# Optimization experiments

Hardware: AMD Instinct MI355X
Metric: run time of the kernel (lower is better)

Reference implementation:

```python
import jax, jax.numpy as jnp
import numpy as np

B, DIM, H, W = 8, 512, 32, 32
NUM_HEADS, KEY_DIM, VALUE_DIM, DIM_OUT = 8, 64, 64, 512


def setup_inputs() -> dict:
    key = jax.random.key(0)
    ks = jax.random.split(key, 5)
    return {
        "x": jax.random.normal(ks[0], (B, DIM, H, W), dtype=jnp.float32),
        "query_proj": jax.random.normal(ks[1], (NUM_HEADS, KEY_DIM, DIM), dtype=jnp.float32),
        "key_proj": jax.random.normal(ks[2], (DIM, KEY_DIM), dtype=jnp.float32),
        "value_proj": jax.random.normal(ks[3], (DIM, VALUE_DIM), dtype=jnp.float32),
        "out_proj": jax.random.normal(ks[4], (DIM_OUT, NUM_HEADS, VALUE_DIM), dtype=jnp.float32),
    }


def reference(x, query_proj, key_proj, value_proj, out_proj):
    b, d, h, w = x.shape
    key_dim = query_proj.shape[1]
    scale = key_dim ** (-0.5)
    # flatten spatial dims to tokens: [b, n, d] where n = h*w (m == x here)
    rx = jnp.transpose(x.reshape(b, d, h * w), (0, 2, 1))
    q = jnp.einsum('bnd,hkd->bnhk', rx, query_proj)
    k = jnp.einsum('bmd,dk->bmk', rx, key_proj)          # single shared K head
    attn = jax.nn.softmax(jnp.einsum('bnhk,bmk->bnhm', q, k) * scale, axis=-1)
    v = jnp.einsum('bmd,dv->bmv', rx, value_proj)        # single shared V head
    o = jnp.einsum('bnhm,bmv->bnhv', attn, v)
    result = jnp.einsum('bnhv,dhv->bdn', o, out_proj)
    return result.reshape(b, -1, h, w)
```

## Files before the change

kernel.cpp:

```cpp
#include <hip/hip_runtime.h>
#include <math.h>

#define BATCH 8
#define DIMD  512
#define NTOK  1024
#define NH    8
#define CQKV  640
#define DOUT  512

typedef __attribute__((ext_vector_type(8))) short short8;
typedef __attribute__((ext_vector_type(4))) short short4v;
typedef __attribute__((ext_vector_type(4))) float f32x4;

__device__ __forceinline__ short bf16rn(float x) {
    unsigned u = __float_as_uint(x);
    u += 0x7FFF + ((u >> 16) & 1);
    return (short)(u >> 16);
}
__device__ __forceinline__ float bf16tof(short s) {
    return __uint_as_float(((unsigned)(unsigned short)s) << 16);
}
struct HL { short h, l; };
__device__ __forceinline__ HL bf16split(float x) {
    HL r;
    r.h = bf16rn(x);
    r.l = bf16rn(x - bf16tof(r.h));
    return r;
}
__device__ __forceinline__ void dma16(const short* g, short* l) {
    __builtin_amdgcn_global_load_lds(
        (const __attribute__((address_space(1))) unsigned int*)g,
        (__attribute__((address_space(3))) unsigned int*)l, 16, 0, 0);
}
__device__ __forceinline__ unsigned packbf2(float f0, float f1) {
    return __builtin_amdgcn_perm(__float_as_uint(f1), __float_as_uint(f0), 0x07060302);
}

#if defined(__has_builtin)
#if __has_builtin(__builtin_amdgcn_mfma_f32_16x16x16bf16_1k)
#define HAVE_MFMA16_BUILTIN 1
__device__ __forceinline__ f32x4 mfma16(short4v a, short4v b, f32x4 c) {
    return __builtin_amdgcn_mfma_f32_16x16x16bf16_1k(a, b, c, 0, 0, 0);
}
#elif __has_builtin(__builtin_amdgcn_mfma_f32_16x16x16_bf16)
#define HAVE_MFMA16_BUILTIN 1
__device__ __forceinline__ f32x4 mfma16(short4v a, short4v b, f32x4 c) {
    return __builtin_amdgcn_mfma_f32_16x16x16_bf16(a, b, c, 0, 0, 0);
}
#endif
#endif
#ifndef HAVE_MFMA16_BUILTIN
__device__ __forceinline__ f32x4 mfma16(short4v a, short4v b, f32x4 c) {
    asm("s_nop 1\n\tv_mfma_f32_16x16x16_bf16 %0, %1, %2, %0"
        : "+v"(c) : "v"(a), "v"(b));
    return c;
}
#endif


__global__ __launch_bounds__(256) void prepack_all(const float* __restrict__ x,
                                                   const float* __restrict__ qp,
                                                   const float* __restrict__ kp,
                                                   const float* __restrict__ vp,
                                                   const float* __restrict__ wout,
                                                   short* __restrict__ whi,
                                                   short* __restrict__ wlo,
                                                   short* __restrict__ xhi,
                                                   short* __restrict__ xlo,
                                                   short* __restrict__ wof) {
    __shared__ float Cs[64][65];
    const int blk = blockIdx.x;
    const int t = threadIdx.x;
    if (blk < 1024) {
        const int nt = blk & 15, dt = (blk >> 4) & 7, b = blk >> 7;
        #pragma unroll
        for (int i = 0; i < 4; ++i) {
            int row = (t >> 4) + i * 16;
            float4 v = *(const float4*)(x + ((size_t)(b * DIMD + dt * 64 + row)) * NTOK
                                          + nt * 64 + (t & 15) * 4);
            Cs[row][(t & 15) * 4 + 0] = v.x;
            Cs[row][(t & 15) * 4 + 1] = v.y;
            Cs[row][(t & 15) * 4 + 2] = v.z;
            Cs[row][(t & 15) * 4 + 3] = v.w;
        }
        __syncthreads();
        for (int u = t; u < 512; u += 256) {
            int lane2 = u & 63, cidx = u >> 6;
            int q2 = lane2 >> 4, r2 = lane2 & 15;
            int kt_loc = cidx & 1, mt_loc = cidx >> 1;
            short8 h8, l8;
            #pragma unroll
            for (int j = 0; j < 8; ++j) {
                HL s = bf16split(Cs[kt_loc * 32 + q2 * 8 + j][mt_loc * 16 + r2]);
                h8[j] = s.h; l8[j] = s.l;
            }
            size_t off = (((size_t)(b * 64 + nt * 4 + mt_loc)) * 16 + dt * 2 + kt_loc) * 512
                         + lane2 * 8;
            *(short8*)&xhi[off] = h8;
            *(short8*)&xlo[off] = l8;
        }
    } else if (blk < 1184) {
        int tid = (blk - 1024) * 256 + t;
        int lane = tid & 63, kt = (tid >> 6) & 15, ct = tid >> 10;
        int q = lane >> 4, r = lane & 15;
        int c = ct * 16 + r;
        short8 h, l;
        #pragma unroll
        for (int j = 0; j < 8; ++j) {
            int d = kt * 32 + q * 8 + j;
            float v;
            if (c < 64)       v = kp[d * 64 + c];
            else if (c < 128) v = vp[d * 64 + (c - 64)];
            else              v = qp[(size_t)(c - 128) * DIMD + d];
            HL s = bf16split(v);
            h[j] = s.h; l[j] = s.l;
        }
        *(short8*)&whi[(size_t)tid * 8] = h;
        *(short8*)&wlo[(size_t)tid * 8] = l;
    } else {
        int tid = (blk - 1184) * 256 + t;
        int lane = tid & 63, kt = (tid >> 6) & 15, mt = tid >> 10;
        int q = lane >> 4, r = lane & 15;
        const float* src = wout + (size_t)(mt * 16 + r) * DOUT + kt * 32 + q * 8;
        short8 h;
        #pragma unroll
        for (int j = 0; j < 8; ++j) h[j] = bf16rn(src[j]);
        *(short8*)&wof[(size_t)tid * 8] = h;
    }
}

__global__ __launch_bounds__(256) void qkv_gemm(const short* __restrict__ xhi,
                                                const short* __restrict__ xlo,
                                                const short* __restrict__ whi,
                                                const short* __restrict__ wlo,
                                                short* __restrict__ khi,
                                                short* __restrict__ klo,
                                                short* __restrict__ vf,
                                                short* __restrict__ qhi,
                                                short* __restrict__ qlo) {
    __shared__ __align__(16) char pool[49152];
    short* Ah = (short*)pool;
    short* Al = Ah + 8192;
    short* Bh = Al + 8192;
    short* Bl = Bh + 4096;
    float (*Cs)[65] = (float(*)[65])pool;

    const int idx = blockIdx.x;
    const int low = idx & 7, rest = idx >> 3;
    const int cb = rest % 10, gh = rest / 10;
    const int g = gh * 8 + low;
    const int b = g >> 3, bml = g & 7;

    const int tid = threadIdx.x, w = tid >> 6, lane = tid & 63;
    const int q = lane >> 4, r = lane & 15;
    f32x4 acc[2][4];
    #pragma unroll
    for (int i = 0; i < 2; ++i)
        #pragma unroll
        for (int j = 0; j < 4; ++j) acc[i][j] = (f32x4){0.f, 0.f, 0.f, 0.f};

    for (int it = 0; it < 8; ++it) {
        __syncthreads();
        for (int u = w; u < 16; u += 4) {
            size_t ga = ((size_t)((b * 64 + bml * 8 + (u >> 1)) * 16 + it * 2 + (u & 1))) * 512 + lane * 8;
            dma16(xhi + ga, &Ah[u * 512]);
            dma16(xlo + ga, &Al[u * 512]);
            if (u < 8) {
                size_t gb = ((size_t)((cb * 4 + (u >> 1)) * 16 + it * 2 + (u & 1))) * 512 + lane * 8;
                dma16(whi + gb, &Bh[u * 512]);
                dma16(wlo + gb, &Bl[u * 512]);
            }
        }
        __syncthreads();
        #pragma unroll
        for (int kc = 0; kc < 2; ++kc) {
            short8 ah[2], al[2];
            #pragma unroll
            for (int rt = 0; rt < 2; ++rt) {
                ah[rt] = *(short8*)&Ah[((w * 2 + rt) * 2 + kc) * 512 + lane * 8];
                al[rt] = *(short8*)&Al[((w * 2 + rt) * 2 + kc) * 512 + lane * 8];
            }
            #pragma unroll
            for (int tt = 0; tt < 4; ++tt) {
                short8 bh = *(short8*)&Bh[(tt * 2 + kc) * 512 + lane * 8];
                short8 bl = *(short8*)&Bl[(tt * 2 + kc) * 512 + lane * 8];
                #pragma unroll
                for (int rt = 0; rt < 2; ++rt) {
                    acc[rt][tt] = __builtin_amdgcn_mfma_f32_16x16x32_bf16(ah[rt], bh, acc[rt][tt], 0, 0, 0);
                    acc[rt][tt] = __builtin_amdgcn_mfma_f32_16x16x32_bf16(ah[rt], bl, acc[rt][tt], 0, 0, 0);
                    acc[rt][tt] = __builtin_amdgcn_mfma_f32_16x16x32_bf16(al[rt], bh, acc[rt][tt], 0, 0, 0);
                }
            }
        }
    }

    __syncthreads();
    #pragma unroll
    for (int rt = 0; rt < 2; ++rt)
        #pragma unroll
        for (int reg = 0; reg < 4; ++reg)
            #pragma unroll
            for (int tt = 0; tt < 4; ++tt)
                Cs[w * 32 + rt * 16 + q * 4 + reg][tt * 16 + r] = acc[rt][tt][reg];
    __syncthreads();

    if (cb == 0) {
        for (int u = tid; u < 1024; u += 256) {
            int lane2 = u & 63, ic = (u >> 6) & 7, tl = u >> 9;
            int q2 = lane2 >> 4, r2 = lane2 & 15;
            int i = ic >> 1, cc = ic & 1;
            short8 h8, l8;
            #pragma unroll
            for (int j = 0; j < 8; ++j) {
                HL s = bf16split(Cs[tl * 64 + i * 16 + r2][cc * 32 + q2 * 8 + j]);
                h8[j] = s.h; l8[j] = s.l;
            }
            size_t off = ((size_t)(b * 16 + bml * 2 + tl) * 8 + ic) * 512 + lane2 * 8;
            *(short8*)&khi[off] = h8;
            *(short8*)&klo[off] = l8;
        }
    } else if (cb == 1) {
        for (int u = tid; u < 1024; u += 256) {
            int a = u & 31, ic = (u >> 5) & 15, tl = u >> 9;
            int c4 = ic >> 2, tv = ic & 3;
            short8 v8;
            #pragma unroll
            for (int jj = 0; jj < 8; ++jj) {
                int lane2 = a * 2 + (jj >> 2), j = jj & 3;
                int qn = lane2 >> 4, r2 = lane2 & 15;
                v8[jj] = bf16rn(Cs[tl * 64 + c4 * 16 + qn * 4 + j][tv * 16 + r2]);
            }
            size_t off = ((size_t)(b * 16 + bml * 2 + tl) * 16 + ic) * 256 + a * 8;
            *(short8*)&vf[off] = v8;
        }
    } else {
        const int hd = cb - 2;
        const float qscale = 0.125f * 1.44269504f;
        for (int u = tid; u < 1024; u += 256) {
            int lane2 = u & 63, ch = u >> 6;
            int q2 = lane2 >> 4, r2 = lane2 & 15;
            int kc = ch & 1, ntl = ch >> 1;
            short8 h8, l8;
            #pragma unroll
            for (int j = 0; j < 8; ++j) {
                HL s = bf16split(Cs[ntl * 16 + r2][kc * 32 + q2 * 8 + j] * qscale);
                h8[j] = s.h; l8[j] = s.l;
            }
            size_t off = ((((size_t)(b * 8 + hd) * 64 + bml * 8 + ntl) * 2 + kc) * 64 + lane2) * 8;
            *(short8*)&qhi[off] = h8;
            *(short8*)&qlo[off] = l8;
        }
    }
}

__global__ __launch_bounds__(256) void attn_mfma(const short* __restrict__ qhi_g,
                                                 const short* __restrict__ qlo_g,
                                                 const short* __restrict__ khi_g,
                                                 const short* __restrict__ klo_g,
                                                 const short* __restrict__ vf_g,
                                                 short* __restrict__ ob) {
    __shared__ short Khi[2][4096], Klo[2][4096], Vf[2][4096];
    const int blk = blockIdx.x;
    const int b   = blk & 7;
    const int h   = (blk >> 3) & 7;
    const int qt  = blk >> 6;
    const int tid = threadIdx.x;
    const int w    = tid >> 6;
    const int lane = tid & 63;
    const int q    = lane >> 4;
    const int r    = lane & 15;

    short8 qhi[2][2], qlo[2][2];
    #pragma unroll
    for (int rt = 0; rt < 2; ++rt) {
        const int nt = qt * 8 + w * 2 + rt;
        #pragma unroll
        for (int c = 0; c < 2; ++c) {
            size_t off = ((((size_t)(b * 8 + h) * 64 + nt) * 2 + c) * 64 + lane) * 8;
            qhi[rt][c] = *(const short8*)&qhi_g[off];
            qlo[rt][c] = *(const short8*)&qlo_g[off];
        }
    }

    short4v bones4;
    #pragma unroll
    for (int j = 0; j < 4; ++j) bones4[j] = (short)0x3F80;

    f32x4 oacc[2][4], lacc[2];
    float m_[2];
    #pragma unroll
    for (int rt = 0; rt < 2; ++rt) {
        #pragma unroll
        for (int tt = 0; tt < 4; ++tt) oacc[rt][tt] = (f32x4){0.f, 0.f, 0.f, 0.f};
        lacc[rt] = (f32x4){0.f, 0.f, 0.f, 0.f};
        m_[rt] = -1e30f;
    }

    const int kbase = lane * 8;
    const int vbase = lane * 4;

    {
        const size_t kb = ((size_t)(b * 16 + 0) * 8) * 512;
        #pragma unroll
        for (int ch0 = 0; ch0 < 2; ++ch0) {
            int ch = w + ch0 * 4;
            dma16(khi_g + kb + ch * 512 + lane * 8, &Khi[0][ch * 512]);
            dma16(klo_g + kb + ch * 512 + lane * 8, &Klo[0][ch * 512]);
            dma16(vf_g  + kb + ch * 512 + lane * 8, &Vf [0][ch * 512]);
        }
    }

    for (int t = 0; t < 16; ++t) {
        const int cur = t & 1;
        __builtin_amdgcn_sched_barrier(0);
        asm volatile("s_waitcnt vmcnt(0) lgkmcnt(0)" ::: "memory");
        __builtin_amdgcn_sched_barrier(0);
        __syncthreads();
        if (t < 15) {
            const size_t kb = ((size_t)(b * 16 + t + 1) * 8) * 512;
            #pragma unroll
            for (int ch0 = 0; ch0 < 2; ++ch0) {
                int ch = w + ch0 * 4;
                dma16(khi_g + kb + ch * 512 + lane * 8, &Khi[cur ^ 1][ch * 512]);
                dma16(klo_g + kb + ch * 512 + lane * 8, &Klo[cur ^ 1][ch * 512]);
                dma16(vf_g  + kb + ch * 512 + lane * 8, &Vf [cur ^ 1][ch * 512]);
            }
        }

        f32x4 sT[2][4];
        #pragma unroll
        for (int rt = 0; rt < 2; ++rt)
            #pragma unroll
            for (int i = 0; i < 4; ++i) sT[rt][i] = (f32x4){0.f, 0.f, 0.f, 0.f};
        #pragma unroll
        for (int cc = 0; cc < 2; ++cc) {
            #pragma unroll
            for (int i = 0; i < 4; ++i) {
                short8 kh = *(short8*)&Khi[cur][(i * 2 + cc) * 512 + kbase];
                short8 kl = *(short8*)&Klo[cur][(i * 2 + cc) * 512 + kbase];
                #pragma unroll
                for (int rt = 0; rt < 2; ++rt) {
                    sT[rt][i] = __builtin_amdgcn_mfma_f32_16x16x32_bf16(kh, qhi[rt][cc], sT[rt][i], 0, 0, 0);
                    sT[rt][i] = __builtin_amdgcn_mfma_f32_16x16x32_bf16(kl, qhi[rt][cc], sT[rt][i], 0, 0, 0);
                    sT[rt][i] = __builtin_amdgcn_mfma_f32_16x16x32_bf16(kh, qlo[rt][cc], sT[rt][i], 0, 0, 0);
                }
            }
        }

        float pm[2];
        #pragma unroll
        for (int rt = 0; rt < 2; ++rt) {
            float a0 = fmaxf(fmaxf(sT[rt][0][0], sT[rt][0][1]), fmaxf(sT[rt][0][2], sT[rt][0][3]));
            float a1 = fmaxf(fmaxf(sT[rt][1][0], sT[rt][1][1]), fmaxf(sT[rt][1][2], sT[rt][1][3]));
            float a2 = fmaxf(fmaxf(sT[rt][2][0], sT[rt][2][1]), fmaxf(sT[rt][2][2], sT[rt][2][3]));
            float a3 = fmaxf(fmaxf(sT[rt][3][0], sT[rt][3][1]), fmaxf(sT[rt][3][2], sT[rt][3][3]));
            pm[rt] = fmaxf(fmaxf(a0, a1), fmaxf(a2, a3));
        }
        bool need = (pm[0] > m_[0] + 30.f) || (pm[1] > m_[1] + 30.f);
        if (__any((int)need)) {
            #pragma unroll
            for (int rt = 0; rt < 2; ++rt) {
                float full = fmaxf(pm[rt], __shfl_xor(pm[rt], 16));
                full = fmaxf(full, __shfl_xor(full, 32));
                float nm = fmaxf(m_[rt], full);
                float alpha = exp2f(m_[rt] - nm);
                m_[rt] = nm;
                #pragma unroll
                for (int reg = 0; reg < 4; ++reg) {
                    float areg = __shfl(alpha, q * 20 + reg);
                    lacc[rt][reg] *= areg;
                    #pragma unroll
                    for (int tt = 0; tt < 4; ++tt) oacc[rt][tt][reg] *= areg;
                }
            }
        }
        #pragma unroll
        for (int rt = 0; rt < 2; ++rt)
            #pragma unroll
            for (int i = 0; i < 4; ++i)
                #pragma unroll
                for (int reg = 0; reg < 4; ++reg)
                    sT[rt][i][reg] = exp2f(sT[rt][i][reg] - m_[rt]);

        #pragma unroll
        for (int c = 0; c < 4; ++c) {
            short4v pf[2];
            #pragma unroll
            for (int rt = 0; rt < 2; ++rt) {
                union { uint2 u; short4v s; } pk;
                pk.u.x = packbf2(sT[rt][c][0], sT[rt][c][1]);
                pk.u.y = packbf2(sT[rt][c][2], sT[rt][c][3]);
                pf[rt] = pk.s;
                lacc[rt] = mfma16(pf[rt], bones4, lacc[rt]);
            }
            #pragma unroll
            for (int tt = 0; tt < 4; ++tt) {
                short4v vfr = *(const short4v*)&Vf[cur][(c * 4 + tt) * 256 + vbase];
                #pragma unroll
                for (int rt = 0; rt < 2; ++rt)
                    oacc[rt][tt] = mfma16(pf[rt], vfr, oacc[rt][tt]);
            }
        }
    }

    asm volatile("s_nop 7\n\ts_nop 7" :::);

    #pragma unroll
    for (int rt = 0; rt < 2; ++rt) {
        const int nt = qt * 8 + w * 2 + rt;
        #pragma unroll
        for (int reg = 0; reg < 4; ++reg) {
            float inv = 1.f / lacc[rt][reg];
            #pragma unroll
            for (int tt = 0; tt < 4; ++tt) {
                int ct = h * 2 + (tt >> 1);
                int lanep = ((tt & 1) * 2 + (r >> 3)) * 16 + q * 4 + reg;
                ob[((((size_t)b * 64 + nt) * 16 + ct) * 64 + lanep) * 8 + (r & 7)] =
                    bf16rn(oacc[rt][tt][reg] * inv);
            }
        }
    }
}

__global__ __launch_bounds__(256) void out_gemm(const short* __restrict__ wof,
                                                const short* __restrict__ obf,
                                                float* __restrict__ out) {
    __shared__ short Ah[2][4096];
    __shared__ short Bh[2][4096];
    const int b = blockIdx.z, bd = blockIdx.y, bn = blockIdx.x;
    const int tid = threadIdx.x, w = tid >> 6, lane = tid & 63;
    const int q = lane >> 4, r = lane & 15;
    f32x4 acc[4];
    #pragma unroll
    for (int j = 0; j < 4; ++j) acc[j] = (f32x4){0.f, 0.f, 0.f, 0.f};

    for (int u = w; u < 8; u += 4) {
        size_t ga = ((size_t)((bd * 4 + (u >> 1)) * 16 + (u & 1))) * 512 + lane * 8;
        dma16(wof + ga, &Ah[0][u * 512]);
        size_t gb = ((size_t)((b * 64 + bn * 4 + (u >> 1)) * 16 + (u & 1))) * 512 + lane * 8;
        dma16(obf + gb, &Bh[0][u * 512]);
    }

    for (int it = 0; it < 8; ++it) {
        const int cur = it & 1;
        __syncthreads();
        if (it < 7) {
            for (int u = w; u < 8; u += 4) {
                size_t ga = ((size_t)((bd * 4 + (u >> 1)) * 16 + (it + 1) * 2 + (u & 1))) * 512 + lane * 8;
                dma16(wof + ga, &Ah[cur ^ 1][u * 512]);
                size_t gb = ((size_t)((b * 64 + bn * 4 + (u >> 1)) * 16 + (it + 1) * 2 + (u & 1))) * 512 + lane * 8;
                dma16(obf + gb, &Bh[cur ^ 1][u * 512]);
            }
        }
        #pragma unroll
        for (int kc = 0; kc < 2; ++kc) {
            short8 a = *(short8*)&Ah[cur][(w * 2 + kc) * 512 + lane * 8];
            #pragma unroll
            for (int tt = 0; tt < 4; ++tt) {
                short8 bb = *(short8*)&Bh[cur][(tt * 2 + kc) * 512 + lane * 8];
                acc[tt] = __builtin_amdgcn_mfma_f32_16x16x32_bf16(a, bb, acc[tt], 0, 0, 0);
            }
        }
    }
    const int d_base = bd * 64 + w * 16;
    #pragma unroll
    for (int reg = 0; reg < 4; ++reg)
        #pragma unroll
        for (int tt = 0; tt < 4; ++tt)
            out[((size_t)b * DOUT + d_base + q * 4 + reg) * NTOK
                + bn * 64 + tt * 16 + r] = acc[tt][reg];
}

extern "C" void kernel_launch(void* const* d_in, const int* in_sizes, int n_in,
                              void* d_out, int out_size, void* d_ws, size_t ws_size,
                              hipStream_t stream) {
    const float* x  = (const float*)d_in[0];
    const float* qp = (const float*)d_in[1];
    const float* kp = (const float*)d_in[2];
    const float* vp = (const float*)d_in[3];
    const float* op = (const float*)d_in[4];
    float* out = (float*)d_out;

    short* Whi = (short*)d_ws;
    short* Wlo = Whi + 327680;
    short* Xhi = Wlo + 327680;
    short* Xlo = Xhi + 4194304;
    short* Qhi = Xlo + 4194304;
    short* Qlo = Qhi + 4194304;
    short* Khi = Qlo + 4194304;
    short* Klo = Khi + 524288;
    short* Vf  = Klo + 524288;
    short* Wof = Vf  + 524288;
    short* Ob  = Xhi;

    prepack_all <<<1312, 256, 0, stream>>>(x, qp, kp, vp, op,
                                           Whi, Wlo, Xhi, Xlo, Wof);
    qkv_gemm    <<<640, 256, 0, stream>>>(Xhi, Xlo, Whi, Wlo,
                                          Khi, Klo, Vf, Qhi, Qlo);
    attn_mfma   <<<512, 256, 0, stream>>>(Qhi, Qlo, Khi, Klo, Vf, Ob);
    out_gemm    <<<dim3(16, 8, BATCH), 256, 0, stream>>>(Wof, Ob, out);
}
```

Measured before the change: 159.6 us.

## Split attention KV range across two wave groups with LDS merge

The attention kernel now runs 512 threads per block: two groups of four waves each process half of the key/value sequence for the same query tiles, each with its own double-buffered LDS stage region. At the end, the second group writes its partial output, row sums and running max to shared memory, and the first group merges them with a rescaled flash-attention combine before writing. This doubles the waves available per block to hide MFMA and memory latency. The cost is an extra LDS round trip, a block-wide sync, and more LDS use per block, which may limit how many blocks can be resident.

```diff
diff --git a/kernel.cpp b/kernel.cpp
--- a/kernel.cpp
+++ b/kernel.cpp
@@ -253,13 +253,16 @@
     }
 }
 
-__global__ __launch_bounds__(256) void attn_mfma(const short* __restrict__ qhi_g,
+__global__ __launch_bounds__(512) void attn_mfma(const short* __restrict__ qhi_g,
                                                  const short* __restrict__ qlo_g,
                                                  const short* __restrict__ khi_g,
                                                  const short* __restrict__ klo_g,
                                                  const short* __restrict__ vf_g,
                                                  short* __restrict__ ob) {
-    __shared__ short Khi[2][4096], Klo[2][4096], Vf[2][4096];
+    __shared__ __align__(16) char pool[49152];
+    short* S0 = (short*)pool;
+    float* Sm = (float*)pool;
+
     const int blk = blockIdx.x;
     const int b   = blk & 7;
     const int h   = (blk >> 3) & 7;
@@ -269,11 +272,13 @@
     const int lane = tid & 63;
     const int q    = lane >> 4;
     const int r    = lane & 15;
+    const int p    = w & 3;
+    const int kh   = w >> 2;
 
     short8 qhi[2][2], qlo[2][2];
     #pragma unroll
     for (int rt = 0; rt < 2; ++rt) {
-        const int nt = qt * 8 + w * 2 + rt;
+        const int nt = qt * 8 + p * 2 + rt;
         #pragma unroll
         for (int c = 0; c < 2; ++c) {
             size_t off = ((((size_t)(b * 8 + h) * 64 + nt) * 2 + c) * 64 + lane) * 8;
@@ -296,53 +301,44 @@
         m_[rt] = -1e30f;
     }
 
-    const int kbase = lane * 8;
-    const int vbase = lane * 4;
-
-    {
-        const size_t kb = ((size_t)(b * 16 + 0) * 8) * 512;
-        #pragma unroll
-        for (int ch0 = 0; ch0 < 2; ++ch0) {
-            int ch = w + ch0 * 4;
-            dma16(khi_g + kb + ch * 512 + lane * 8, &Khi[0][ch * 512]);
-            dma16(klo_g + kb + ch * 512 + lane * 8, &Klo[0][ch * 512]);
-            dma16(vf_g  + kb + ch * 512 + lane * 8, &Vf [0][ch * 512]);
-        }
-    }
-
-    for (int t = 0; t < 16; ++t) {
-        const int cur = t & 1;
+    #define STAGE(u_, buf_) {                                                   \
+        int t_ = kh * 8 + ((u_) >> 1), s_ = (u_) & 1;                           \
+        short* reg_ = S0 + (kh * 2 + (buf_)) * 6144;                            \
+        size_t kb_ = ((size_t)((b * 16 + t_) * 8 + s_ * 4 + p)) * 512 + lane * 8; \
+        dma16(khi_g + kb_, reg_ + p * 512);                                     \
+        dma16(klo_g + kb_, reg_ + 2048 + p * 512);                              \
+        size_t vb_ = ((size_t)((b * 16 + t_) * 16 + s_ * 8 + p * 2)) * 256 + lane * 8; \
+        dma16(vf_g + vb_, reg_ + 4096 + p * 512);                               \
+    }
+
+    STAGE(0, 0);
+
+    for (int u = 0; u < 16; ++u) {
+        const int cur = u & 1;
         __builtin_amdgcn_sched_barrier(0);
         asm volatile("s_waitcnt vmcnt(0) lgkmcnt(0)" ::: "memory");
         __builtin_amdgcn_sched_barrier(0);
         __syncthreads();
-        if (t < 15) {
-            const size_t kb = ((size_t)(b * 16 + t + 1) * 8) * 512;
-            #pragma unroll
-            for (int ch0 = 0; ch0 < 2; ++ch0) {
-                int ch = w + ch0 * 4;
-                dma16(khi_g + kb + ch * 512 + lane * 8, &Khi[cur ^ 1][ch * 512]);
-                dma16(klo_g + kb + ch * 512 + lane * 8, &Klo[cur ^ 1][ch * 512]);
-                dma16(vf_g  + kb + ch * 512 + lane * 8, &Vf [cur ^ 1][ch * 512]);
-            }
-        }
-
-        f32x4 sT[2][4];
+        if (u < 15) STAGE(u + 1, cur ^ 1);
+
+        const short* reg = S0 + (kh * 2 + cur) * 6144;
+
+        f32x4 sT[2][2];
         #pragma unroll
         for (int rt = 0; rt < 2; ++rt)
             #pragma unroll
-            for (int i = 0; i < 4; ++i) sT[rt][i] = (f32x4){0.f, 0.f, 0.f, 0.f};
+            for (int i2 = 0; i2 < 2; ++i2) sT[rt][i2] = (f32x4){0.f, 0.f, 0.f, 0.f};
         #pragma unroll
         for (int cc = 0; cc < 2; ++cc) {
             #pragma unroll
-            for (int i = 0; i < 4; ++i) {
-                short8 kh = *(short8*)&Khi[cur][(i * 2 + cc) * 512 + kbase];
-                short8 kl = *(short8*)&Klo[cur][(i * 2 + cc) * 512 + kbase];
+            for (int i2 = 0; i2 < 2; ++i2) {
+                short8 kh8 = *(short8*)&reg[(i2 * 2 + cc) * 512 + lane * 8];
+                short8 kl8 = *(short8*)&reg[2048 + (i2 * 2 + cc) * 512 + lane * 8];
                 #pragma unroll
                 for (int rt = 0; rt < 2; ++rt) {
-                    sT[rt][i] = __builtin_amdgcn_mfma_f32_16x16x32_bf16(kh, qhi[rt][cc], sT[rt][i], 0, 0, 0);
-                    sT[rt][i] = __builtin_amdgcn_mfma_f32_16x16x32_bf16(kl, qhi[rt][cc], sT[rt][i], 0, 0, 0);
-                    sT[rt][i] = __builtin_amdgcn_mfma_f32_16x16x32_bf16(kh, qlo[rt][cc], sT[rt][i], 0, 0, 0);
+                    sT[rt][i2] = __builtin_amdgcn_mfma_f32_16x16x32_bf16(kh8, qhi[rt][cc], sT[rt][i2], 0, 0, 0);
+                    sT[rt][i2] = __builtin_amdgcn_mfma_f32_16x16x32_bf16(kl8, qhi[rt][cc], sT[rt][i2], 0, 0, 0);
+                    sT[rt][i2] = __builtin_amdgcn_mfma_f32_16x16x32_bf16(kh8, qlo[rt][cc], sT[rt][i2], 0, 0, 0);
                 }
             }
         }
@@ -352,9 +348,7 @@
         for (int rt = 0; rt < 2; ++rt) {
             float a0 = fmaxf(fmaxf(sT[rt][0][0], sT[rt][0][1]), fmaxf(sT[rt][0][2], sT[rt][0][3]));
             float a1 = fmaxf(fmaxf(sT[rt][1][0], sT[rt][1][1]), fmaxf(sT[rt][1][2], sT[rt][1][3]));
-            float a2 = fmaxf(fmaxf(sT[rt][2][0], sT[rt][2][1]), fmaxf(sT[rt][2][2], sT[rt][2][3]));
-            float a3 = fmaxf(fmaxf(sT[rt][3][0], sT[rt][3][1]), fmaxf(sT[rt][3][2], sT[rt][3][3]));
-            pm[rt] = fmaxf(fmaxf(a0, a1), fmaxf(a2, a3));
+            pm[rt] = fmaxf(a0, a1);
         }
         bool need = (pm[0] > m_[0] + 30.f) || (pm[1] > m_[1] + 30.f);
         if (__any((int)need)) {
@@ -366,57 +360,88 @@
                 float alpha = exp2f(m_[rt] - nm);
                 m_[rt] = nm;
                 #pragma unroll
-                for (int reg = 0; reg < 4; ++reg) {
-                    float areg = __shfl(alpha, q * 20 + reg);
-                    lacc[rt][reg] *= areg;
+                for (int reg2 = 0; reg2 < 4; ++reg2) {
+                    float areg = __shfl(alpha, q * 20 + reg2);
+                    lacc[rt][reg2] *= areg;
                     #pragma unroll
-                    for (int tt = 0; tt < 4; ++tt) oacc[rt][tt][reg] *= areg;
+                    for (int tt = 0; tt < 4; ++tt) oacc[rt][tt][reg2] *= areg;
                 }
             }
         }
         #pragma unroll
         for (int rt = 0; rt < 2; ++rt)
             #pragma unroll
-            for (int i = 0; i < 4; ++i)
+            for (int i2 = 0; i2 < 2; ++i2)
                 #pragma unroll
-                for (int reg = 0; reg < 4; ++reg)
-                    sT[rt][i][reg] = exp2f(sT[rt][i][reg] - m_[rt]);
-
-        #pragma unroll
-        for (int c = 0; c < 4; ++c) {
+                for (int reg2 = 0; reg2 < 4; ++reg2)
+                    sT[rt][i2][reg2] = exp2f(sT[rt][i2][reg2] - m_[rt]);
+
+        #pragma unroll
+        for (int c2 = 0; c2 < 2; ++c2) {
             short4v pf[2];
             #pragma unroll
             for (int rt = 0; rt < 2; ++rt) {
                 union { uint2 u; short4v s; } pk;
-                pk.u.x = packbf2(sT[rt][c][0], sT[rt][c][1]);
-                pk.u.y = packbf2(sT[rt][c][2], sT[rt][c][3]);
+                pk.u.x = packbf2(sT[rt][c2][0], sT[rt][c2][1]);
+                pk.u.y = packbf2(sT[rt][c2][2], sT[rt][c2][3]);
                 pf[rt] = pk.s;
                 lacc[rt] = mfma16(pf[rt], bones4, lacc[rt]);
             }
             #pragma unroll
             for (int tt = 0; tt < 4; ++tt) {
-                short4v vfr = *(const short4v*)&Vf[cur][(c * 4 + tt) * 256 + vbase];
+                short4v vfr = *(const short4v*)&reg[4096 + (c2 * 4 + tt) * 256 + lane * 4];
                 #pragma unroll
                 for (int rt = 0; rt < 2; ++rt)
                     oacc[rt][tt] = mfma16(pf[rt], vfr, oacc[rt][tt]);
             }
         }
     }
-
+    #undef STAGE
+
+    __builtin_amdgcn_sched_barrier(0);
+    asm volatile("s_waitcnt vmcnt(0) lgkmcnt(0)" ::: "memory");
+    __builtin_amdgcn_sched_barrier(0);
+    __syncthreads();
     asm volatile("s_nop 7\n\ts_nop 7" :::);
 
-    #pragma unroll
-    for (int rt = 0; rt < 2; ++rt) {
-        const int nt = qt * 8 + w * 2 + rt;
-        #pragma unroll
-        for (int reg = 0; reg < 4; ++reg) {
-            float inv = 1.f / lacc[rt][reg];
-            #pragma unroll
-            for (int tt = 0; tt < 4; ++tt) {
-                int ct = h * 2 + (tt >> 1);
-                int lanep = ((tt & 1) * 2 + (r >> 3)) * 16 + q * 4 + reg;
-                ob[((((size_t)b * 64 + nt) * 16 + ct) * 64 + lanep) * 8 + (r & 7)] =
-                    bf16rn(oacc[rt][tt][reg] * inv);
+    float* st = Sm + ((size_t)(p * 64 + lane)) * 44;
+    if (kh == 1) {
+        #pragma unroll
+        for (int rt = 0; rt < 2; ++rt) {
+            #pragma unroll
+            for (int tt = 0; tt < 4; ++tt)
+                *(f32x4*)&st[rt * 16 + tt * 4] = oacc[rt][tt];
+            *(f32x4*)&st[32 + rt * 4] = lacc[rt];
+            st[40 + rt] = m_[rt];
+        }
+    }
+    __syncthreads();
+    if (kh == 0) {
+        #pragma unroll
+        for (int rt = 0; rt < 2; ++rt) {
+            const int nt = qt * 8 + p * 2 + rt;
+            float mB = st[40 + rt];
+            float nm = fmaxf(m_[rt], mB);
+            float aA = exp2f(m_[rt] - nm);
+            float aB = exp2f(mB - nm);
+            f32x4 lB = *(f32x4*)&st[32 + rt * 4];
+            f32x4 oB[4];
+            #pragma unroll
+            for (int tt = 0; tt < 4; ++tt) oB[tt] = *(f32x4*)&st[rt * 16 + tt * 4];
+            #pragma unroll
+            for (int reg2 = 0; reg2 < 4; ++reg2) {
+                float aAr = __shfl(aA, q * 20 + reg2);
+                float aBr = __shfl(aB, q * 20 + reg2);
+                float l = aAr * lacc[rt][reg2] + aBr * lB[reg2];
+                float inv = 1.f / l;
+                #pragma unroll
+                for (int tt = 0; tt < 4; ++tt) {
+                    float o = aAr * oacc[rt][tt][reg2] + aBr * oB[tt][reg2];
+                    int ct = h * 2 + (tt >> 1);
+                    int lanep = ((tt & 1) * 2 + (r >> 3)) * 16 + q * 4 + reg2;
+                    ob[((((size_t)b * 64 + nt) * 16 + ct) * 64 + lanep) * 8 + (r & 7)] =
+                        bf16rn(o * inv);
+                }
             }
         }
     }
@@ -497,6 +522,6 @@
                                            Whi, Wlo, Xhi, Xlo, Wof);
     qkv_gemm    <<<640, 256, 0, stream>>>(Xhi, Xlo, Whi, Wlo,
                                           Khi, Klo, Vf, Qhi, Qlo);
-    attn_mfma   <<<512, 256, 0, stream>>>(Qhi, Qlo, Khi, Klo, Vf, Ob);
+    attn_mfma   <<<512, 512, 0, stream>>>(Qhi, Qlo, Khi, Klo, Vf, Ob);
     out_gemm    <<<dim3(16, 8, BATCH), 256, 0, stream>>>(Wof, Ob, out);
 }
```

Result: slower. 165.8 us (+3.9%).
